# Kernel optimization log

Hardware: AMD Instinct MI355X
Metric: run time of the kernel (lower is better)

## Reference

```python
import jax, jax.numpy as jnp
import numpy as np

MIDC = 256
HEADS = 16
HEADC = MIDC // HEADS
EPS = 1e-5


def _layernorm(x, w, b):
    # Faithful to the custom torch LayerNorm: unbiased std (ddof=1) and
    # division by (std + eps), NOT sqrt(var + eps).
    mean = jnp.mean(x, axis=-1, keepdims=True)
    std = jnp.std(x, axis=-1, keepdims=True, ddof=1)
    return w * (x - mean) / (std + EPS) + b


def setup_inputs() -> dict:
    key = jax.random.key(0)
    ks = jax.random.split(key, 3)
    B, HW = 8, 16384
    x = jax.random.normal(ks[0], (B, HW, MIDC), dtype=jnp.float32)
    W_qkv = jax.random.normal(ks[1], (3 * MIDC, MIDC), dtype=jnp.float32) * 0.02
    b_qkv = jnp.zeros((3 * MIDC,), dtype=jnp.float32)
    kln_w = jnp.ones((HEADS, 1, HEADC), dtype=jnp.float32)
    kln_b = jnp.zeros((HEADS, 1, HEADC), dtype=jnp.float32)
    vln_w = jnp.ones((HEADS, 1, HEADC), dtype=jnp.float32)
    vln_b = jnp.zeros((HEADS, 1, HEADC), dtype=jnp.float32)
    W_proj = jax.random.normal(ks[2], (MIDC, MIDC), dtype=jnp.float32) * 0.02
    b_proj = jnp.zeros((MIDC,), dtype=jnp.float32)
    return {"x": x, "W_qkv": W_qkv, "b_qkv": b_qkv,
            "kln_w": kln_w, "kln_b": kln_b, "vln_w": vln_w, "vln_b": vln_b,
            "W_proj": W_proj, "b_proj": b_proj}


def reference(x, W_qkv, b_qkv, kln_w, kln_b, vln_w, vln_b, W_proj, b_proj):
    B, HW, C = x.shape
    bias = x
    # QKV projection -> [B, heads, HW, 3*headc]
    qkv = (jnp.einsum('bnc,oc->bno', x, W_qkv) + b_qkv)
    qkv = qkv.reshape(B, HW, HEADS, 3 * HEADC).transpose(0, 2, 1, 3)
    q, k, v = jnp.split(qkv, 3, axis=-1)  # each [B, heads, HW, headc]
    k = _layernorm(k, kln_w, kln_b)
    v = _layernorm(v, vln_w, vln_b)
    # linear attention: kv = k^T v / HW, then q @ kv
    kv = jnp.einsum('bhnd,bhne->bhde', k, v) / HW  # [B, heads, headc, headc]
    out = jnp.einsum('bhnd,bhde->bhne', q, kv)     # [B, heads, HW, headc]
    out = out.transpose(0, 2, 1, 3).reshape(B, HW, C)
    ret = out + bias
    proj = jnp.einsum('bnc,oc->bno', ret, W_proj) + b_proj
    return jax.nn.gelu(proj, approximate=False) + bias
```

## Files before the change

### kernel.cpp

```cpp
#include <hip/hip_runtime.h>
#include <hip/hip_bf16.h>
#include <math.h>


#define EPSF 1e-5f

typedef __bf16 bf16x8 __attribute__((ext_vector_type(8)));
typedef __bf16 bf16x4 __attribute__((ext_vector_type(4)));
typedef float  f32x4  __attribute__((ext_vector_type(4)));

__global__ void k0_prep(const float* __restrict__ Wqkv, const float* __restrict__ Wproj,
                        __bf16* __restrict__ Wkv, __bf16* __restrict__ Wp,
                        float* __restrict__ kv8) {
  int idx = blockIdx.x * 256 + threadIdx.x;
  kv8[idx] = 0.f;
  if (idx < 131072) {
    int r = idx >> 8, c = idx & 255;
    int half = r >> 8;
    int rr = r & 255;
    int h = rr >> 4, d = rr & 15;
    Wkv[idx] = (__bf16)Wqkv[(h*48 + 16 + half*16 + d)*256 + c];
  }
  if (idx < 65536) Wp[idx] = (__bf16)Wproj[idx];
}

__launch_bounds__(512, 4)
__global__ void k1a(const float* __restrict__ x, const __bf16* __restrict__ Wkv,
                    const float* __restrict__ bqkv,
                    const float* __restrict__ klnw, const float* __restrict__ klnb,
                    const float* __restrict__ vlnw, const float* __restrict__ vlnb,
                    float* __restrict__ kv8) {
  __shared__ __align__(16) char smem[70656];
  __bf16 (*xs)[264] = reinterpret_cast<__bf16(*)[264]>(smem);
  const int tid = threadIdx.x;
  const int w = tid >> 6, l = tid & 63, lr = l & 15, g = l >> 4;
  __bf16 (*tTk)[72] = reinterpret_cast<__bf16(*)[72]>(smem + 33792 + w*4608);
  __bf16 (*tTv)[64] = reinterpret_cast<__bf16(*)[64]>(smem + w*4096);

  const long row0 = (long)blockIdx.x * 64;
  const int b = (int)(row0 >> 14);

  #pragma unroll
  for (int i = 0; i < 8; ++i) {
    int idx = tid + i*512;
    int r = idx >> 6, c4 = (idx & 63) << 2;
    f32x4 v = *reinterpret_cast<const f32x4*>(x + (row0 + r)*256 + c4);
    bf16x4 pk; pk[0]=(__bf16)v[0]; pk[1]=(__bf16)v[1]; pk[2]=(__bf16)v[2]; pk[3]=(__bf16)v[3];
    *reinterpret_cast<bf16x4*>(&xs[r][c4]) = pk;
  }
  __syncthreads();

  f32x4 acc[4][4];
  for (int s=0;s<4;s++) for (int rb=0;rb<4;rb++)
    for (int j=0;j<4;j++) acc[s][rb][j]=0.f;
  #pragma unroll
  for (int kc = 0; kc < 8; ++kc) {
    const int kb = kc*32 + g*8;
    bf16x8 wfr[4], bf_[4];
    #pragma unroll
    for (int s=0;s<4;s++) {
      const int wrow = ((s>>1)<<8) + w*32 + ((s&1)<<4) + lr;
      wfr[s] = *reinterpret_cast<const bf16x8*>(Wkv + (size_t)wrow*256 + kb);
    }
    #pragma unroll
    for (int rb=0;rb<4;rb++)
      bf_[rb] = *reinterpret_cast<const bf16x8*>(&xs[rb*16+lr][kb]);
    #pragma unroll
    for (int s=0;s<4;s++)
      #pragma unroll
      for (int rb=0;rb<4;rb++)
        acc[s][rb] = __builtin_amdgcn_mfma_f32_16x16x32_bf16(wfr[s], bf_[rb], acc[s][rb], 0,0,0);
  }

  #pragma unroll
  for (int s=0;s<2;s++) {
    const int h = 2*w + s;
    const f32x4 bb  = *reinterpret_cast<const f32x4*>(bqkv + h*48 + 16 + 4*g);
    const f32x4 lwv = *reinterpret_cast<const f32x4*>(klnw + h*16 + 4*g);
    const f32x4 lbv = *reinterpret_cast<const f32x4*>(klnb + h*16 + 4*g);
    #pragma unroll
    for (int rb=0;rb<4;rb++) {
      float v0 = acc[s][rb][0] + bb[0];
      float v1 = acc[s][rb][1] + bb[1];
      float v2 = acc[s][rb][2] + bb[2];
      float v3 = acc[s][rb][3] + bb[3];
      float sum = v0+v1+v2+v3;
      sum += __shfl_xor(sum, 16); sum += __shfl_xor(sum, 32);
      const float mu = sum * 0.0625f;
      const float d0=v0-mu, d1=v1-mu, d2=v2-mu, d3=v3-mu;
      float q = d0*d0 + d1*d1 + d2*d2 + d3*d3;
      q += __shfl_xor(q, 16); q += __shfl_xor(q, 32);
      const float sc = __frsqrt_rn(q * (1.f/15.f));
      const int rr = rb*16 + lr;
      tTk[s*16 + 4*g+0][rr] = (__bf16)(lwv[0]*d0*sc + lbv[0]);
      tTk[s*16 + 4*g+1][rr] = (__bf16)(lwv[1]*d1*sc + lbv[1]);
      tTk[s*16 + 4*g+2][rr] = (__bf16)(lwv[2]*d2*sc + lbv[2]);
      tTk[s*16 + 4*g+3][rr] = (__bf16)(lwv[3]*d3*sc + lbv[3]);
    }
  }
  __syncthreads();

  #pragma unroll
  for (int s=2;s<4;s++) {
    const int cbl = s - 2;
    const int h = 2*w + cbl;
    const f32x4 bb  = *reinterpret_cast<const f32x4*>(bqkv + h*48 + 32 + 4*g);
    const f32x4 lwv = *reinterpret_cast<const f32x4*>(vlnw + h*16 + 4*g);
    const f32x4 lbv = *reinterpret_cast<const f32x4*>(vlnb + h*16 + 4*g);
    #pragma unroll
    for (int rb=0;rb<4;rb++) {
      float v0 = acc[s][rb][0] + bb[0];
      float v1 = acc[s][rb][1] + bb[1];
      float v2 = acc[s][rb][2] + bb[2];
      float v3 = acc[s][rb][3] + bb[3];
      float sum = v0+v1+v2+v3;
      sum += __shfl_xor(sum, 16); sum += __shfl_xor(sum, 32);
      const float mu = sum * 0.0625f;
      const float d0=v0-mu, d1=v1-mu, d2=v2-mu, d3=v3-mu;
      float q = d0*d0 + d1*d1 + d2*d2 + d3*d3;
      q += __shfl_xor(q, 16); q += __shfl_xor(q, 32);
      const float sc = __frsqrt_rn(q * (1.f/15.f));
      const int rr = rb*16 + lr;
      tTv[cbl*16 + 4*g+0][rr ^ (((4*g+0)&7)<<3)] = (__bf16)(lwv[0]*d0*sc + lbv[0]);
      tTv[cbl*16 + 4*g+1][rr ^ (((4*g+1)&7)<<3)] = (__bf16)(lwv[1]*d1*sc + lbv[1]);
      tTv[cbl*16 + 4*g+2][rr ^ (((4*g+2)&7)<<3)] = (__bf16)(lwv[2]*d2*sc + lbv[2]);
      tTv[cbl*16 + 4*g+3][rr ^ (((4*g+3)&7)<<3)] = (__bf16)(lwv[3]*d3*sc + lbv[3]);
    }
  }

  float* slice = kv8 + (size_t)(blockIdx.x & 7) * 32768;
  #pragma unroll
  for (int hh=0; hh<2; ++hh) {
    f32x4 c; c[0]=0.f; c[1]=0.f; c[2]=0.f; c[3]=0.f;
    #pragma unroll
    for (int ch=0; ch<2; ++ch) {
      const int s = ch*32 + g*8;
      bf16x8 a  = *reinterpret_cast<const bf16x8*>(&tTk[hh*16 + lr][s]);
      bf16x8 bv = *reinterpret_cast<const bf16x8*>(&tTv[hh*16 + lr][s ^ ((lr&7)<<3)]);
      c = __builtin_amdgcn_mfma_f32_16x16x32_bf16(a, bv, c, 0,0,0);
    }
    float* dst = slice + ((size_t)(b*16 + 2*w + hh) << 8);
    #pragma unroll
    for (int j=0;j<4;j++)
      atomicAdd(dst + (4*g+j)*16 + lr, c[j]);
  }
}

__global__ void k2_weff(const float* __restrict__ Wqkv, const float* __restrict__ bqkv,
                        const float* __restrict__ kv8,
                        __bf16* __restrict__ Wqe, float* __restrict__ beff) {
  const int b = blockIdx.x >> 4, h = blockIdx.x & 15;
  const int c = threadIdx.x;
  __shared__ float kvs[16][16];
  float acc0 = 0.f;
  #pragma unroll
  for (int s=0;s<8;s++) acc0 += kv8[(size_t)s*32768 + (b*16 + h)*256 + c];
  kvs[c >> 4][c & 15] = acc0 * (1.f/16384.f);
  __syncthreads();
  #pragma unroll 4
  for (int e=0;e<16;e++) {
    float acc = 0.f;
    #pragma unroll
    for (int d=0; d<16; d++)
      acc += kvs[d][e] * Wqkv[(h*48 + d)*256 + c];
    Wqe[((size_t)b*256 + h*16 + e)*256 + c] = (__bf16)acc;
  }
  if (c < 16) {
    float acc = 0.f;
    #pragma unroll
    for (int d=0; d<16; d++) acc += kvs[d][c] * bqkv[h*48 + d];
    beff[b*256 + h*16 + c] = acc;
  }
}

__launch_bounds__(512, 4)
__global__ void k3_fused(const float* __restrict__ x, const __bf16* __restrict__ Wqe,
                         const float* __restrict__ beff, const __bf16* __restrict__ Wp,
                         const float* __restrict__ bproj, float* __restrict__ out) {
  __shared__ __align__(16) __bf16 xs[64][264];
  __shared__ __align__(16) char rsraw[33792];
  __bf16 (*rs)[264] = reinterpret_cast<__bf16(*)[264]>(rsraw);
  float  (*fst)[260] = reinterpret_cast<float(*)[260]>(rsraw);
  const int tid = threadIdx.x;
  const long browg = (long)blockIdx.x * 64;
  const int b = (int)(browg >> 14);
  const int w = tid>>6, l = tid&63, lr = l&15, g = l>>4;

  #pragma unroll
  for (int i = 0; i < 8; ++i) {
    int idx = tid + i*512;
    int r = idx >> 6, c4 = (idx & 63) << 2;
    f32x4 v = *reinterpret_cast<const f32x4*>(x + (browg + r)*256 + c4);
    bf16x4 pk; pk[0]=(__bf16)v[0]; pk[1]=(__bf16)v[1]; pk[2]=(__bf16)v[2]; pk[3]=(__bf16)v[3];
    *reinterpret_cast<bf16x4*>(&xs[r][c4]) = pk;
  }

  const __bf16* Bq = Wqe + (size_t)b*65536;
  bf16x8 wq[2][8];
  #pragma unroll
  for (int cb=0;cb<2;cb++) {
    const __bf16* wp = Bq + (size_t)(w*32 + cb*16 + lr)*256 + g*8;
    #pragma unroll
    for (int kc=0;kc<8;kc++) wq[cb][kc] = *reinterpret_cast<const bf16x8*>(wp + kc*32);
  }
  __syncthreads();

  f32x4 acc[2][4];
  for (int cb=0;cb<2;cb++) for (int rb=0;rb<4;rb++)
    for (int j=0;j<4;j++) acc[cb][rb][j]=0.f;
  #pragma unroll
  for (int kc=0;kc<8;kc++) {
    const int kb = kc*32 + g*8;
    bf16x8 bf_[4];
    #pragma unroll
    for (int rb=0;rb<4;rb++)
      bf_[rb] = *reinterpret_cast<const bf16x8*>(&xs[rb*16+lr][kb]);
    #pragma unroll
    for (int cb=0;cb<2;cb++)
      #pragma unroll
      for (int rb=0;rb<4;rb++)
        acc[cb][rb] = __builtin_amdgcn_mfma_f32_16x16x32_bf16(wq[cb][kc], bf_[rb], acc[cb][rb], 0,0,0);
  }

  bf16x8 wpj[2][8];
  #pragma unroll
  for (int cb=0;cb<2;cb++) {
    const __bf16* wp = Wp + (size_t)(w*32 + cb*16 + lr)*256 + g*8;
    #pragma unroll
    for (int kc=0;kc<8;kc++) wpj[cb][kc] = *reinterpret_cast<const bf16x8*>(wp + kc*32);
  }

  #pragma unroll
  for (int cb=0;cb<2;cb++) {
    const int c0 = w*32 + cb*16 + 4*g;
    const f32x4 be = *reinterpret_cast<const f32x4*>(beff + b*256 + c0);
    #pragma unroll
    for (int rb=0;rb<4;rb++) {
      const int r = rb*16 + lr;
      bf16x4 xv = *reinterpret_cast<const bf16x4*>(&xs[r][c0]);
      bf16x4 pk;
      #pragma unroll
      for (int j=0;j<4;j++)
        pk[j] = (__bf16)(acc[cb][rb][j] + be[j] + (float)xv[j]);
      *reinterpret_cast<bf16x4*>(&rs[r][c0]) = pk;
    }
  }
  __syncthreads();

  f32x4 acc2[2][4];
  for (int cb=0;cb<2;cb++) for (int rb=0;rb<4;rb++)
    for (int j=0;j<4;j++) acc2[cb][rb][j]=0.f;
  #pragma unroll
  for (int kc=0;kc<8;kc++) {
    const int kb = kc*32 + g*8;
    bf16x8 bf_[4];
    #pragma unroll
    for (int rb=0;rb<4;rb++)
      bf_[rb] = *reinterpret_cast<const bf16x8*>(&rs[rb*16+lr][kb]);
    #pragma unroll
    for (int cb=0;cb<2;cb++)
      #pragma unroll
      for (int rb=0;rb<4;rb++)
        acc2[cb][rb] = __builtin_amdgcn_mfma_f32_16x16x32_bf16(wpj[cb][kc], bf_[rb], acc2[cb][rb], 0,0,0);
  }
  __syncthreads();

  #pragma unroll
  for (int half=0; half<2; ++half) {
    #pragma unroll
    for (int cb=0;cb<2;cb++) {
      const int c0 = w*32 + cb*16 + 4*g;
      const f32x4 bp4 = *reinterpret_cast<const f32x4*>(bproj + c0);
      #pragma unroll
      for (int rbh=0;rbh<2;rbh++) {
        const int rb = half*2 + rbh;
        const int r = rb*16 + lr;
        bf16x4 xv = *reinterpret_cast<const bf16x4*>(&xs[r][c0]);
        f32x4 o;
        #pragma unroll
        for (int j=0;j<4;j++) {
          float z = acc2[cb][rb][j] + bp4[j];
          o[j] = 0.5f*z*(1.f + erff(z*0.70710678118f)) + (float)xv[j];
        }
        *reinterpret_cast<f32x4*>(&fst[r - half*32][c0]) = o;
      }
    }
    __syncthreads();
    #pragma unroll
    for (int i=0;i<4;i++) {
      int idx = tid + i*512;
      int r32 = idx >> 6, c4 = (idx & 63) << 2;
      f32x4 v = *reinterpret_cast<const f32x4*>(&fst[r32][c4]);
      *reinterpret_cast<f32x4*>(out + (browg + half*32 + r32)*256 + c4) = v;
    }
    if (half == 0) __syncthreads();
  }
}

extern "C" void kernel_launch(void* const* d_in, const int* in_sizes, int n_in,
                              void* d_out, int out_size, void* d_ws, size_t ws_size,
                              hipStream_t stream) {
  const float* x    = (const float*)d_in[0];
  const float* Wqkv = (const float*)d_in[1];
  const float* bqkv = (const float*)d_in[2];
  const float* klnw = (const float*)d_in[3];
  const float* klnb = (const float*)d_in[4];
  const float* vlnw = (const float*)d_in[5];
  const float* vlnb = (const float*)d_in[6];
  const float* Wproj= (const float*)d_in[7];
  const float* bproj= (const float*)d_in[8];
  float* out = (float*)d_out;

  char* ws = (char*)d_ws;
  __bf16* Wkv = (__bf16*)(ws);
  __bf16* Wp  = (__bf16*)(ws + 262144);
  __bf16* Wqe = (__bf16*)(ws + 393216);
  float*  beff= (float*) (ws + 1441792);

  float* kv8 = (float*)d_out;

  k0_prep <<<1024, 256, 0, stream>>>(Wqkv, Wproj, Wkv, Wp, kv8);
  k1a     <<<2048, 512, 0, stream>>>(x, Wkv, bqkv, klnw, klnb, vlnw, vlnb, kv8);
  k2_weff <<<128, 256, 0, stream>>>(Wqkv, bqkv, kv8, Wqe, beff);
  k3_fused<<<2048, 512, 0, stream>>>(x, Wqe, beff, Wp, bproj, out);
}
```

Baseline: 193.4 us.

## Replace kv atomics with per-block partials and shrink k1a shared memory

k1a no longer atomically adds its per-head k^T v tile into eight sliced accumulators. Each block now writes its own partial tile to a scratch buffer in the output, and k2_weff sums 256 partials per (batch, head) with four independent accumulators. The K/V layernorm staging is reorganised so both tiles of a head share a compact per-wave LDS region. This cuts LDS from about 70KB to 33KB per block, which may allow more blocks per CU, and removes the zeroing pass from k0_prep. The cost is a larger partial buffer, 2048*16*256 floats, plus a longer serial reduction in the small k2 kernel.

```diff
diff --git a/kernel.cpp b/kernel.cpp
--- a/kernel.cpp
+++ b/kernel.cpp
@@ -10,11 +10,9 @@
 typedef float  f32x4  __attribute__((ext_vector_type(4)));
 
 __global__ void k0_prep(const float* __restrict__ Wqkv, const float* __restrict__ Wproj,
-                        __bf16* __restrict__ Wkv, __bf16* __restrict__ Wp,
-                        float* __restrict__ kv8) {
+                        __bf16* __restrict__ Wkv, __bf16* __restrict__ Wp) {
   int idx = blockIdx.x * 256 + threadIdx.x;
-  kv8[idx] = 0.f;
-  if (idx < 131072) {
+  {
     int r = idx >> 8, c = idx & 255;
     int half = r >> 8;
     int rr = r & 255;
@@ -29,16 +27,13 @@
                     const float* __restrict__ bqkv,
                     const float* __restrict__ klnw, const float* __restrict__ klnb,
                     const float* __restrict__ vlnw, const float* __restrict__ vlnb,
-                    float* __restrict__ kv8) {
-  __shared__ __align__(16) char smem[70656];
+                    float* __restrict__ part) {
+  __shared__ __align__(16) char smem[33792];
   __bf16 (*xs)[264] = reinterpret_cast<__bf16(*)[264]>(smem);
   const int tid = threadIdx.x;
   const int w = tid >> 6, l = tid & 63, lr = l & 15, g = l >> 4;
-  __bf16 (*tTk)[72] = reinterpret_cast<__bf16(*)[72]>(smem + 33792 + w*4608);
-  __bf16 (*tTv)[64] = reinterpret_cast<__bf16(*)[64]>(smem + w*4096);
 
   const long row0 = (long)blockIdx.x * 64;
-  const int b = (int)(row0 >> 14);
 
   #pragma unroll
   for (int i = 0; i < 8; ++i) {
@@ -71,91 +66,70 @@
       for (int rb=0;rb<4;rb++)
         acc[s][rb] = __builtin_amdgcn_mfma_f32_16x16x32_bf16(wfr[s], bf_[rb], acc[s][rb], 0,0,0);
   }
-
-  #pragma unroll
-  for (int s=0;s<2;s++) {
-    const int h = 2*w + s;
-    const f32x4 bb  = *reinterpret_cast<const f32x4*>(bqkv + h*48 + 16 + 4*g);
-    const f32x4 lwv = *reinterpret_cast<const f32x4*>(klnw + h*16 + 4*g);
-    const f32x4 lbv = *reinterpret_cast<const f32x4*>(klnb + h*16 + 4*g);
-    #pragma unroll
-    for (int rb=0;rb<4;rb++) {
-      float v0 = acc[s][rb][0] + bb[0];
-      float v1 = acc[s][rb][1] + bb[1];
-      float v2 = acc[s][rb][2] + bb[2];
-      float v3 = acc[s][rb][3] + bb[3];
-      float sum = v0+v1+v2+v3;
-      sum += __shfl_xor(sum, 16); sum += __shfl_xor(sum, 32);
-      const float mu = sum * 0.0625f;
-      const float d0=v0-mu, d1=v1-mu, d2=v2-mu, d3=v3-mu;
-      float q = d0*d0 + d1*d1 + d2*d2 + d3*d3;
-      q += __shfl_xor(q, 16); q += __shfl_xor(q, 32);
-      const float sc = __frsqrt_rn(q * (1.f/15.f));
-      const int rr = rb*16 + lr;
-      tTk[s*16 + 4*g+0][rr] = (__bf16)(lwv[0]*d0*sc + lbv[0]);
-      tTk[s*16 + 4*g+1][rr] = (__bf16)(lwv[1]*d1*sc + lbv[1]);
-      tTk[s*16 + 4*g+2][rr] = (__bf16)(lwv[2]*d2*sc + lbv[2]);
-      tTk[s*16 + 4*g+3][rr] = (__bf16)(lwv[3]*d3*sc + lbv[3]);
-    }
-  }
-  __syncthreads();
-
-  #pragma unroll
-  for (int s=2;s<4;s++) {
-    const int cbl = s - 2;
-    const int h = 2*w + cbl;
-    const f32x4 bb  = *reinterpret_cast<const f32x4*>(bqkv + h*48 + 32 + 4*g);
-    const f32x4 lwv = *reinterpret_cast<const f32x4*>(vlnw + h*16 + 4*g);
-    const f32x4 lbv = *reinterpret_cast<const f32x4*>(vlnb + h*16 + 4*g);
-    #pragma unroll
-    for (int rb=0;rb<4;rb++) {
-      float v0 = acc[s][rb][0] + bb[0];
-      float v1 = acc[s][rb][1] + bb[1];
-      float v2 = acc[s][rb][2] + bb[2];
-      float v3 = acc[s][rb][3] + bb[3];
-      float sum = v0+v1+v2+v3;
-      sum += __shfl_xor(sum, 16); sum += __shfl_xor(sum, 32);
-      const float mu = sum * 0.0625f;
-      const float d0=v0-mu, d1=v1-mu, d2=v2-mu, d3=v3-mu;
-      float q = d0*d0 + d1*d1 + d2*d2 + d3*d3;
-      q += __shfl_xor(q, 16); q += __shfl_xor(q, 32);
-      const float sc = __frsqrt_rn(q * (1.f/15.f));
-      const int rr = rb*16 + lr;
-      tTv[cbl*16 + 4*g+0][rr ^ (((4*g+0)&7)<<3)] = (__bf16)(lwv[0]*d0*sc + lbv[0]);
-      tTv[cbl*16 + 4*g+1][rr ^ (((4*g+1)&7)<<3)] = (__bf16)(lwv[1]*d1*sc + lbv[1]);
-      tTv[cbl*16 + 4*g+2][rr ^ (((4*g+2)&7)<<3)] = (__bf16)(lwv[2]*d2*sc + lbv[2]);
-      tTv[cbl*16 + 4*g+3][rr ^ (((4*g+3)&7)<<3)] = (__bf16)(lwv[3]*d3*sc + lbv[3]);
-    }
-  }
-
-  float* slice = kv8 + (size_t)(blockIdx.x & 7) * 32768;
+  __syncthreads();
+
+  char* pw = smem + w*4096;
+
   #pragma unroll
   for (int hh=0; hh<2; ++hh) {
-    f32x4 c; c[0]=0.f; c[1]=0.f; c[2]=0.f; c[3]=0.f;
+    const int h = 2*w + hh;
+    #pragma unroll
+    for (int kv=0; kv<2; ++kv) {
+      const int s = kv*2 + hh;
+      const f32x4 bb  = *reinterpret_cast<const f32x4*>(bqkv + h*48 + 16 + kv*16 + 4*g);
+      const f32x4 lwv = *reinterpret_cast<const f32x4*>((kv ? vlnw : klnw) + h*16 + 4*g);
+      const f32x4 lbv = *reinterpret_cast<const f32x4*>((kv ? vlnb : klnb) + h*16 + 4*g);
+      char* tile = pw + kv*2048;
+      #pragma unroll
+      for (int rb=0;rb<4;rb++) {
+        float v0 = acc[s][rb][0] + bb[0];
+        float v1 = acc[s][rb][1] + bb[1];
+        float v2 = acc[s][rb][2] + bb[2];
+        float v3 = acc[s][rb][3] + bb[3];
+        float sum = v0+v1+v2+v3;
+        sum += __shfl_xor(sum, 16); sum += __shfl_xor(sum, 32);
+        const float mu = sum * 0.0625f;
+        const float d0=v0-mu, d1=v1-mu, d2=v2-mu, d3=v3-mu;
+        float q = d0*d0 + d1*d1 + d2*d2 + d3*d3;
+        q += __shfl_xor(q, 16); q += __shfl_xor(q, 32);
+        const float sc = __frsqrt_rn(q * (1.f/15.f));
+        const int cb = (2*rb + (lr>>3))*256 + ((lr&7)<<1);
+        *reinterpret_cast<__bf16*>(tile + cb + (4*g+0)*16) = (__bf16)(lwv[0]*d0*sc + lbv[0]);
+        *reinterpret_cast<__bf16*>(tile + cb + (4*g+1)*16) = (__bf16)(lwv[1]*d1*sc + lbv[1]);
+        *reinterpret_cast<__bf16*>(tile + cb + (4*g+2)*16) = (__bf16)(lwv[2]*d2*sc + lbv[2]);
+        *reinterpret_cast<__bf16*>(tile + cb + (4*g+3)*16) = (__bf16)(lwv[3]*d3*sc + lbv[3]);
+      }
+    }
+    f32x4 c0; c0[0]=0.f; c0[1]=0.f; c0[2]=0.f; c0[3]=0.f;
     #pragma unroll
     for (int ch=0; ch<2; ++ch) {
-      const int s = ch*32 + g*8;
-      bf16x8 a  = *reinterpret_cast<const bf16x8*>(&tTk[hh*16 + lr][s]);
-      bf16x8 bv = *reinterpret_cast<const bf16x8*>(&tTv[hh*16 + lr][s ^ ((lr&7)<<3)]);
-      c = __builtin_amdgcn_mfma_f32_16x16x32_bf16(a, bv, c, 0,0,0);
-    }
-    float* dst = slice + ((size_t)(b*16 + 2*w + hh) << 8);
+      bf16x8 a  = *reinterpret_cast<const bf16x8*>(pw +        (ch*4+g)*256 + lr*16);
+      bf16x8 bv = *reinterpret_cast<const bf16x8*>(pw + 2048 + (ch*4+g)*256 + lr*16);
+      c0 = __builtin_amdgcn_mfma_f32_16x16x32_bf16(a, bv, c0, 0,0,0);
+    }
+    float* dst = part + ((size_t)blockIdx.x*16 + h)*256;
     #pragma unroll
     for (int j=0;j<4;j++)
-      atomicAdd(dst + (4*g+j)*16 + lr, c[j]);
+      dst[(4*g+j)*16 + lr] = c0[j];
   }
 }
 
 __global__ void k2_weff(const float* __restrict__ Wqkv, const float* __restrict__ bqkv,
-                        const float* __restrict__ kv8,
+                        const float* __restrict__ part,
                         __bf16* __restrict__ Wqe, float* __restrict__ beff) {
   const int b = blockIdx.x >> 4, h = blockIdx.x & 15;
   const int c = threadIdx.x;
   __shared__ float kvs[16][16];
-  float acc0 = 0.f;
-  #pragma unroll
-  for (int s=0;s<8;s++) acc0 += kv8[(size_t)s*32768 + (b*16 + h)*256 + c];
-  kvs[c >> 4][c & 15] = acc0 * (1.f/16384.f);
+  const float* base = part + ((size_t)(b*256)*16 + h)*256 + c;
+  float a0=0.f, a1=0.f, a2=0.f, a3=0.f;
+  #pragma unroll 8
+  for (int i=0;i<256;i+=4) {
+    a0 += base[(size_t)(i+0)*4096];
+    a1 += base[(size_t)(i+1)*4096];
+    a2 += base[(size_t)(i+2)*4096];
+    a3 += base[(size_t)(i+3)*4096];
+  }
+  kvs[c >> 4][c & 15] = ((a0+a1)+(a2+a3)) * (1.f/16384.f);
   __syncthreads();
   #pragma unroll 4
   for (int e=0;e<16;e++) {
@@ -317,10 +291,10 @@
   __bf16* Wqe = (__bf16*)(ws + 393216);
   float*  beff= (float*) (ws + 1441792);
 
-  float* kv8 = (float*)d_out;
-
-  k0_prep <<<1024, 256, 0, stream>>>(Wqkv, Wproj, Wkv, Wp, kv8);
-  k1a     <<<2048, 512, 0, stream>>>(x, Wkv, bqkv, klnw, klnb, vlnw, vlnb, kv8);
-  k2_weff <<<128, 256, 0, stream>>>(Wqkv, bqkv, kv8, Wqe, beff);
+  float* part = (float*)d_out;
+
+  k0_prep <<<512, 256, 0, stream>>>(Wqkv, Wproj, Wkv, Wp);
+  k1a     <<<2048, 512, 0, stream>>>(x, Wkv, bqkv, klnw, klnb, vlnw, vlnb, part);
+  k2_weff <<<128, 256, 0, stream>>>(Wqkv, bqkv, part, Wqe, beff);
   k3_fused<<<2048, 512, 0, stream>>>(x, Wqe, beff, Wp, bproj, out);
 }
```

New measurement: 212.1 us. +9.7%, slower.
